# Performance work log

Hardware: AMD Instinct MI355X
Metric: run time of the kernel (lower is better)

## Reference

```python
import jax, jax.numpy as jnp
import numpy as np

T, H, I, E, K = 4096, 2048, 1408, 8, 2


def setup_inputs() -> dict:
    key = jax.random.key(0)
    k1, k2, k3, k4, k5 = jax.random.split(key, 5)
    hidden_states = jax.random.normal(k1, (T, H), dtype=jnp.float32)
    w13 = jax.random.normal(k2, (E, 2 * I, H), dtype=jnp.float32) * 0.02
    w2 = jax.random.normal(k3, (E, H, I), dtype=jnp.float32) * 0.02
    topk_ids = jax.random.randint(k4, (T, K), 0, E, dtype=jnp.int32)
    topk_weights = jax.random.uniform(k5, (T, K), dtype=jnp.float32)
    return {
        "hidden_states": hidden_states,
        "w13": w13,
        "w2": w2,
        "topk_ids": topk_ids,
        "topk_weights": topk_weights,
    }


def reference(hidden_states, w13, w2, topk_ids, topk_weights):
    # hidden_states: [T, H]; w13: [E, 2I, H]; w2: [E, H, I]
    # topk_ids/topk_weights: [T, K]. local_expert_start = 0.
    num_tokens, hidden = hidden_states.shape
    num_experts = w13.shape[0]
    inter = w13.shape[1] // 2
    gate_w = w13[:, :inter, :]  # [E, I, H]
    up_w = w13[:, inter:, :]    # [E, I, H]

    # Dense per-expert gate/up projections (vectorized grouped GEMM).
    gate = jnp.einsum('th,eih->tei', hidden_states, gate_w)
    up = jnp.einsum('th,eih->tei', hidden_states, up_w)
    act = jax.nn.silu(gate) * up  # [T, E, I]

    # Scatter topk weights into a dense [T, E] routing matrix (zero elsewhere),
    # which reproduces the trivial impl's per-slot weighted accumulation.
    tok = jnp.arange(num_tokens, dtype=jnp.int32)[:, None]
    routing = jnp.zeros((num_tokens, num_experts), dtype=hidden_states.dtype)
    routing = routing.at[tok, topk_ids].add(topk_weights)

    # Weighted combine through the down projection; weighting act first avoids
    # materializing a [T, E, H] intermediate.
    act_w = act * routing[:, :, None]  # [T, E, I]
    out = jnp.einsum('tei,ehi->th', act_w, w2)  # [T, H]
    return out
```

## Files before the change

kernel.cpp:

```cpp
#include <hip/hip_runtime.h>
#include <hip/hip_bf16.h>

#define T_TOK 4096
#define HID   2048
#define INTER 1408
#define TWO_I 2816
#define NEXP  8
#define ROWCAP 9216

#define N8_HS  1048576
#define N8_W13 5767168
#define NCVT   ((N8_HS + N8_W13) / 256)

#define NJOBS1 1408
#define NJOBS2 1024

using bf16x8 = __attribute__((ext_vector_type(8))) __bf16;
using f32x4  = __attribute__((ext_vector_type(4))) float;

__device__ __forceinline__ unsigned short f2bf(float f) {
  unsigned u = __float_as_uint(f);
  u += 0x7fffu + ((u >> 16) & 1u);
  return (unsigned short)(u >> 16);
}

__device__ __forceinline__ void gload16(const void* g, void* l) {
  __builtin_amdgcn_global_load_lds(
      (const __attribute__((address_space(1))) void*)g,
      (__attribute__((address_space(3))) void*)l, 16, 0, 0);
}

__device__ __forceinline__ uint4 pack8(float4 a, float4 b) {
  union { unsigned short us[8]; uint4 v; } o;
  o.us[0] = f2bf(a.x); o.us[1] = f2bf(a.y); o.us[2] = f2bf(a.z); o.us[3] = f2bf(a.w);
  o.us[4] = f2bf(b.x); o.us[5] = f2bf(b.y); o.us[6] = f2bf(b.z); o.us[7] = f2bf(b.w);
  return o.v;
}

__global__ void cvt2route_kernel(const float* __restrict__ hs_f, unsigned short* __restrict__ hs_b,
                                 const float* __restrict__ w13_f, unsigned short* __restrict__ w13_b,
                                 const int* __restrict__ ids, const float* __restrict__ wts,
                                 float* __restrict__ R, int* __restrict__ counts) {
  int bid = blockIdx.x;
  if (bid >= NCVT) {
    int t = (bid - NCVT) * 256 + threadIdx.x;
    if (t >= T_TOK) return;
    int e0 = ids[t * 2], e1 = ids[t * 2 + 1];
    float w0 = wts[t * 2], w1 = wts[t * 2 + 1];
#pragma unroll
    for (int ee = 0; ee < NEXP; ++ee) {
      float r = (e0 == ee ? w0 : 0.0f) + (e1 == ee ? w1 : 0.0f);
      R[t * NEXP + ee] = r;
    }
    atomicAdd(&counts[e0], 1);
    if (e1 != e0) atomicAdd(&counts[e1], 1);
    return;
  }
  int i = bid * 256 + threadIdx.x;
  const float4* p;
  uint4* o;
  int j;
  if (i < N8_HS) {
    p = reinterpret_cast<const float4*>(hs_f);
    o = reinterpret_cast<uint4*>(hs_b);
    j = i;
  } else {
    p = reinterpret_cast<const float4*>(w13_f);
    o = reinterpret_cast<uint4*>(w13_b);
    j = i - N8_HS;
  }
  o[j] = pack8(p[j * 2], p[j * 2 + 1]);
}

__global__ void offsets_kernel(const int* __restrict__ counts,
                               int* __restrict__ offs, int* __restrict__ cursor,
                               int* __restrict__ tl) {
  if (threadIdx.x == 0) {
    int o = 0;
    for (int e = 0; e < NEXP; ++e) {
      offs[e] = o;
      cursor[e] = o;
      o += (counts[e] + 127) & ~127;
    }
    offs[NEXP] = o;
  }
  for (int i = threadIdx.x; i < ROWCAP; i += 256) tl[i] = -1;
}

__global__ void scatter_kernel(const int* __restrict__ ids,
                               int* __restrict__ cursor, int* __restrict__ tl,
                               int* __restrict__ inv) {
  int t = blockIdx.x * 256 + threadIdx.x;
  if (t >= T_TOK) return;
  int e0 = ids[t * 2], e1 = ids[t * 2 + 1];
  int p = atomicAdd(&cursor[e0], 1);
  tl[p] = t;
  inv[t * 2] = p;
  if (e1 != e0) {
    p = atomicAdd(&cursor[e1], 1);
    tl[p] = t;
    inv[t * 2 + 1] = p;
  } else {
    inv[t * 2 + 1] = -1;
  }
}


#define BARR do { __asm__ __volatile__("" ::: "memory"); \
                  __builtin_amdgcn_s_barrier();           \
                  __asm__ __volatile__("" ::: "memory"); } while (0)
#define VMC(n) __asm__ __volatile__("s_waitcnt vmcnt(" #n ")" ::: "memory")

#define STG(P, h, kt, slotOff, hOff)                                        \
  do {                                                                      \
    gload16(P[h][0] + (kt) * 128, smem + (slotOff) + (hOff) + chA);         \
    gload16(P[h][1] + (kt) * 128, smem + (slotOff) + (hOff) + chA + 1024);  \
  } while (0)

#define LDA(dst, S, aq)                                                     \
  do {                                                                      \
    _Pragma("unroll") for (int mi = 0; mi < 4; ++mi) {                      \
      const char* _p = smem + (S) + wmOff + ((aq) * 64 + mi * 16 + l15) * 128; \
      dst[mi][0] = *(const bf16x8*)(_p + ko0);                              \
      dst[mi][1] = *(const bf16x8*)(_p + ko1);                              \
    }                                                                       \
  } while (0)

#define LDB(dst, S, bq)                                                     \
  do {                                                                      \
    _Pragma("unroll") for (int ni = 0; ni < 2; ++ni) {                      \
      const char* _p = smem + (S) + 32768 + wnhOff +                        \
                       (wn1 * 64 + ((bq) * 2 + ni) * 16 + l15) * 128;       \
      dst[ni][0] = *(const bf16x8*)(_p + ko0);                              \
      dst[ni][1] = *(const bf16x8*)(_p + ko1);                              \
    }                                                                       \
  } while (0)

#define MFQ(A, B, aq, bq)                                                   \
  do {                                                                      \
    __builtin_amdgcn_s_setprio(1);                                          \
    _Pragma("unroll") for (int mi = 0; mi < 4; ++mi)                        \
    _Pragma("unroll") for (int ni = 0; ni < 2; ++ni) {                      \
      acc[(aq) * 4 + mi][(bq) * 2 + ni] = __builtin_amdgcn_mfma_f32_16x16x32_bf16( \
          A[mi][0], B[ni][0], acc[(aq) * 4 + mi][(bq) * 2 + ni], 0, 0, 0);  \
      acc[(aq) * 4 + mi][(bq) * 2 + ni] = __builtin_amdgcn_mfma_f32_16x16x32_bf16( \
          A[mi][1], B[ni][1], acc[(aq) * 4 + mi][(bq) * 2 + ni], 0, 0, 0);  \
    }                                                                       \
    __builtin_amdgcn_s_setprio(0);                                          \
  } while (0)

#define EIGHT_PHASES(NIT_, NL_LIM_)                                         \
  for (int i = 0; i < (NIT_); ++i) {                                        \
    const int t0 = 2 * i, t1 = t0 + 1;                                      \
    const bool nl = (i < (NL_LIM_));                                        \
                                                                    \
    LDA(a_lo, 0, 0);                                                        \
    LDB(b_lo, 0, 0);                                                        \
    STG(aS, 0, t1, 65536, 0);                                               \
    BARR; MFQ(a_lo, b_lo, 0, 0); BARR;                                      \
                                                                    \
    LDB(b_hi, 0, 1);                                                        \
    STG(aS, 1, t1, 65536, 16384);                                           \
    BARR; MFQ(a_lo, b_hi, 0, 1); BARR;                                      \
                                                                    \
    LDA(a_hi, 0, 1);                                                        \
    if (nl) STG(bS, 0, t0 + 2, 0, 32768);                                   \
    BARR; MFQ(a_hi, b_hi, 1, 1); BARR;                                      \
                                                                    \
    if (nl) STG(bS, 1, t0 + 2, 0, 49152);                                   \
    BARR; MFQ(a_hi, b_lo, 1, 0);                                            \
    if (nl) { VMC(4); } else { VMC(0); }                                    \
    BARR;                                                                   \
                                                                    \
    LDA(a_lo, 65536, 0);                                                    \
    LDB(b_lo, 65536, 0);                                                    \
    if (nl) STG(aS, 0, t0 + 2, 0, 0);                                       \
    BARR; MFQ(a_lo, b_lo, 0, 0); BARR;                                      \
                                                                    \
    LDB(b_hi, 65536, 1);                                                    \
    if (nl) STG(aS, 1, t0 + 2, 0, 16384);                                   \
    BARR; MFQ(a_lo, b_hi, 0, 1); BARR;                                      \
                                                                    \
    LDA(a_hi, 65536, 1);                                                    \
    if (nl) STG(bS, 0, t1 + 2, 65536, 32768);                               \
    BARR; MFQ(a_hi, b_hi, 1, 1); BARR;                                      \
                                                                    \
    if (nl) STG(bS, 1, t1 + 2, 65536, 49152);                               \
    BARR; MFQ(a_hi, b_lo, 1, 0);                                            \
    if (nl) VMC(4);                                                         \
    BARR;                                                                   \
  }

#define PROLOGUE_STAGE()                                                    \
  do {                                                                      \
    STG(aS, 0, 0, 0, 0);                                                    \
    STG(aS, 1, 0, 0, 16384);                                                \
    STG(bS, 0, 0, 0, 32768);                                                \
    STG(bS, 1, 0, 0, 49152);                                                \
    STG(bS, 0, 1, 65536, 32768);                                            \
    STG(bS, 1, 1, 65536, 49152);                                            \
    VMC(4);                                                                 \
    BARR;                                                                   \
  } while (0)

__global__ __launch_bounds__(512, 2) void gemm1_kernel(
    const unsigned short* __restrict__ hs,
    const unsigned short* __restrict__ w13,
    unsigned short* __restrict__ act,
    const int* __restrict__ tl, const int* __restrict__ offs,
    const float* __restrict__ w2f, unsigned short* __restrict__ w2b,
    int* __restrict__ qcnt) {
  const int tid = threadIdx.x;

  {
    const float4* p = reinterpret_cast<const float4*>(w2f);
    uint4* o = reinterpret_cast<uint4*>(w2b);
    int gid = blockIdx.x * 512 + tid;
#pragma unroll
    for (int q = 0; q < 22; ++q) {
      int idx = q * 131072 + gid;
      o[idx] = pack8(p[idx * 2], p[idx * 2 + 1]);
    }
  }

  __shared__ __align__(16) char smem[131072];
  __shared__ int sjob;

  const int lane = tid & 63, wave = tid >> 6;
  const int wm = wave >> 2, wn = wave & 3;
  const int l15 = lane & 15;
  const int srow = lane >> 3;
  const int scolswz = ((lane & 7) * 16) ^ (srow << 4);
  const int chA = wave * 2048;
  const int wmOff = wm * 16384;
  const int wnhOff = (wn >> 1) * 16384;
  const int wn1 = wn & 1;
  const int rsw = (lane & 7) << 4;
  const int ko0 = ((lane >> 4) * 16) ^ rsw;
  const int ko1 = (64 + (lane >> 4) * 16) ^ rsw;

  const char* hs_b = (const char*)hs;

  for (;;) {
    if (tid == 0) sjob = atomicAdd(qcnt, 1);
    __syncthreads();
    const int job = sjob;
    __syncthreads();
    if (job >= NJOBS1) break;

    const int e = job / 176;
    const int rem = job - e * 176;
    const int by = rem / 11;
    const int bx = rem - by * 11;

    const int rbeg = offs[e], rend = offs[e + 1];
    const int m0 = rbeg + by * 256;
    if (m0 >= rend) continue;
    const int n0 = bx * 128;

    const char* w13_b = (const char*)w13 + (size_t)e * (TWO_I * HID * 2);

    const char* aS[2][2];
    const char* bS[2][2];
#pragma unroll
    for (int h = 0; h < 2; ++h)
#pragma unroll
      for (int it = 0; it < 2; ++it) {
        int rl = h * 128 + (wave * 2 + it) * 8 + srow;
        int grow = m0 + rl;
        int tk = (grow < rend) ? tl[grow] : 0;
        if (tk < 0) tk = 0;
        aS[h][it] = hs_b + (size_t)tk * 4096 + scolswz;
        int wg = rl >> 6, sub = rl & 63;
        int srcB = (sub < 32) ? (n0 + wg * 32 + sub)
                              : (INTER + n0 + wg * 32 + (sub - 32));
        bS[h][it] = w13_b + (size_t)srcB * 4096 + scolswz;
      }

    f32x4 acc[8][4] = {};
    bf16x8 a_lo[4][2], a_hi[4][2], b_lo[2][2], b_hi[2][2];

    PROLOGUE_STAGE();
    EIGHT_PHASES(16, 15);

    const bool okst = (wm == 0) || (rend - m0 >= 256);
    if (okst) {
#pragma unroll
      for (int MI = 0; MI < 8; ++MI)
#pragma unroll
        for (int j = 0; j < 4; ++j) {
          int row = m0 + wm * 128 + MI * 16 + (lane >> 4) * 4 + j;
          size_t base = (size_t)row * INTER + n0 + wn * 32;
#pragma unroll
          for (int NI = 0; NI < 2; ++NI) {
            float g = acc[MI][NI][j], u = acc[MI][NI + 2][j];
            float s = (g / (1.0f + __expf(-g))) * u;
            act[base + NI * 16 + l15] = f2bf(s);
          }
        }
    }
  }
}

__global__ __launch_bounds__(512, 2) void gemm2_kernel(
    const unsigned short* __restrict__ act,
    const unsigned short* __restrict__ w2,
    const float* __restrict__ R, const int* __restrict__ tl,
    const int* __restrict__ offs, unsigned short* __restrict__ partial,
    int* __restrict__ qcnt) {
  const int tid = threadIdx.x;

  __shared__ __align__(16) char smem[131072];
  __shared__ int sjob;

  const int lane = tid & 63, wave = tid >> 6;
  const int wm = wave >> 2, wn = wave & 3;
  const int l15 = lane & 15;
  const int srow = lane >> 3;
  const int scolswz = ((lane & 7) * 16) ^ (srow << 4);
  const int chA = wave * 2048;
  const int wmOff = wm * 16384;
  const int wnhOff = (wn >> 1) * 16384;
  const int wn1 = wn & 1;
  const int rsw = (lane & 7) << 4;
  const int ko0 = ((lane >> 4) * 16) ^ rsw;
  const int ko1 = (64 + (lane >> 4) * 16) ^ rsw;

  const char* act_b = (const char*)act;

  for (;;) {
    if (tid == 0) sjob = atomicAdd(qcnt, 1);
    __syncthreads();
    const int job = sjob;
    __syncthreads();
    if (job >= NJOBS2) break;

    const int e = job >> 7;
    const int rem = job & 127;
    const int by = rem >> 3;
    const int bx = rem & 7;

    const int rbeg = offs[e], rend = offs[e + 1];
    const int m0 = rbeg + by * 256;
    if (m0 >= rend) continue;
    const int n0 = bx * 256;

    const char* w2_b = (const char*)w2 + (size_t)e * (HID * INTER * 2);

    const char* aS[2][2];
    const char* bS[2][2];
#pragma unroll
    for (int h = 0; h < 2; ++h)
#pragma unroll
      for (int it = 0; it < 2; ++it) {
        int rl = h * 128 + (wave * 2 + it) * 8 + srow;
        int grow = m0 + rl;
        if (grow >= rend) grow = rbeg;
        aS[h][it] = act_b + (size_t)grow * (INTER * 2) + scolswz;
        bS[h][it] = w2_b + (size_t)(n0 + rl) * (INTER * 2) + scolswz;
      }

    f32x4 acc[8][4] = {};
    bf16x8 a_lo[4][2], a_hi[4][2], b_lo[2][2], b_hi[2][2];

    PROLOGUE_STAGE();
    EIGHT_PHASES(11, 10);

    const bool okst = (wm == 0) || (rend - m0 >= 256);
    if (okst) {
#pragma unroll
      for (int MI = 0; MI < 8; ++MI) {
        float sc[4];
#pragma unroll
        for (int j = 0; j < 4; ++j) {
          int row = m0 + wm * 128 + MI * 16 + (lane >> 4) * 4 + j;
          int t = tl[row];
          sc[j] = t >= 0 ? R[t * NEXP + e] : 0.0f;
        }
#pragma unroll
        for (int NI = 0; NI < 4; ++NI) {
          int col = n0 + wn * 64 + NI * 16 + l15;
#pragma unroll
          for (int j = 0; j < 4; ++j) {
            int row = m0 + wm * 128 + MI * 16 + (lane >> 4) * 4 + j;
            partial[(size_t)row * HID + col] = f2bf(acc[MI][NI][j] * sc[j]);
          }
        }
      }
    }
  }
}

__global__ void combine_kernel(const unsigned short* __restrict__ P,
                               const int* __restrict__ inv,
                               float* __restrict__ out) {
  int idx = blockIdx.x * 256 + threadIdx.x;
  int t = idx >> 8;
  int c = (idx & 255) << 3;
  int p0 = inv[t * 2], p1 = inv[t * 2 + 1];
  union { uint4 v; unsigned short us[8]; } a, b;
  a.v = *(const uint4*)(P + (size_t)p0 * HID + c);
  float f[8];
#pragma unroll
  for (int j = 0; j < 8; ++j) f[j] = __uint_as_float((unsigned)a.us[j] << 16);
  if (p1 >= 0) {
    b.v = *(const uint4*)(P + (size_t)p1 * HID + c);
#pragma unroll
    for (int j = 0; j < 8; ++j) f[j] += __uint_as_float((unsigned)b.us[j] << 16);
  }
  float4 lo = {f[0], f[1], f[2], f[3]}, hi = {f[4], f[5], f[6], f[7]};
  *(float4*)(out + (size_t)t * HID + c) = lo;
  *(float4*)(out + (size_t)t * HID + c + 4) = hi;
}

extern "C" void kernel_launch(void* const* d_in, const int* in_sizes, int n_in,
                              void* d_out, int out_size, void* d_ws, size_t ws_size,
                              hipStream_t stream) {
  const float* hs_f  = (const float*)d_in[0];
  const float* w13_f = (const float*)d_in[1];
  const float* w2_f  = (const float*)d_in[2];
  const int*   ids   = (const int*)d_in[3];
  const float* wts   = (const float*)d_in[4];
  float* out = (float*)d_out;
  char* ws = (char*)d_ws;

  unsigned short* hs_b  = (unsigned short*)(ws);
  unsigned short* w13_b = (unsigned short*)(ws + 16777216);
  unsigned short* w2_b  = (unsigned short*)(ws + 109051904);
  unsigned short* act   = (unsigned short*)(ws + 155189248);
  float* R              = (float*)(ws + 181141504);
  int*   tl             = (int*)(ws + 181272576);
  int*   inv            = (int*)(ws + 181309440);
  int*   meta           = (int*)(ws + 181342208);
  unsigned short* partial = (unsigned short*)(ws + 16777216);
  int* counts = meta;
  int* offs   = meta + 8;
  int* cursor = meta + 17;
  int* q1     = meta + 26;
  int* q2     = meta + 27;

  hipMemsetAsync(meta, 0, 32 * sizeof(int), stream);

  cvt2route_kernel<<<dim3(NCVT + 16), dim3(256), 0, stream>>>(
      hs_f, hs_b, w13_f, w13_b, ids, wts, R, counts);

  offsets_kernel<<<dim3(1), dim3(256), 0, stream>>>(counts, offs, cursor, tl);
  scatter_kernel<<<dim3(T_TOK / 256), dim3(256), 0, stream>>>(ids, cursor, tl, inv);

  gemm1_kernel<<<dim3(256), dim3(512), 0, stream>>>(hs_b, w13_b, act, tl, offs, w2_f, w2_b, q1);
  gemm2_kernel<<<dim3(256), dim3(512), 0, stream>>>(act, w2_b, R, tl, offs, partial, q2);
  combine_kernel<<<dim3(T_TOK * (HID / 8) / 256), dim3(256), 0, stream>>>(partial, inv, out);
}
```

Before: 356.3 us.

## Use per-expert work queues and defer w2 conversion to tail of gemm1

Replaces the single global job counter in both grouped GEMMs with eight per-expert queues sized from the actual routed row counts. Each block starts on the queue for its blockIdx and moves to the next expert once that queue is empty, so empty tiles are never dequeued and blocks sharing an expert reuse its weights in cache. The fp32-to-bf16 conversion of w2 moves from the start of gemm1 into a dynamically claimed tail loop, so blocks that finish GEMM work early fill the load-imbalance gap. Costs are extra atomics when a queue runs dry and w2 conversion possibly running late in gemm1.

```diff
diff --git a/kernel.cpp b/kernel.cpp
--- a/kernel.cpp
+++ b/kernel.cpp
@@ -12,8 +12,7 @@
 #define N8_W13 5767168
 #define NCVT   ((N8_HS + N8_W13) / 256)
 
-#define NJOBS1 1408
-#define NJOBS2 1024
+#define W2_CHUNKS 704
 
 using bf16x8 = __attribute__((ext_vector_type(8))) __bf16;
 using f32x4  = __attribute__((ext_vector_type(4))) float;
@@ -203,28 +202,39 @@
     BARR;                                                                   \
   } while (0)
 
+#define QPOP(QARR)                                                          \
+  do {                                                                      \
+    if (tid == 0) {                                                         \
+      int got = -1;                                                         \
+      while (qsel < 8) {                                                    \
+        int qe = (myx + qsel) & 7;                                          \
+        int j = atomicAdd(&QARR[qe], 1);                                    \
+        if (j < scap[qe]) { got = (qe << 8) | j; break; }                   \
+        ++qsel;                                                             \
+      }                                                                     \
+      sjob = got;                                                           \
+    }                                                                       \
+    __syncthreads();                                                        \
+  } while (0)
+
 __global__ __launch_bounds__(512, 2) void gemm1_kernel(
     const unsigned short* __restrict__ hs,
     const unsigned short* __restrict__ w13,
     unsigned short* __restrict__ act,
     const int* __restrict__ tl, const int* __restrict__ offs,
     const float* __restrict__ w2f, unsigned short* __restrict__ w2b,
-    int* __restrict__ qcnt) {
+    int* __restrict__ q1, int* __restrict__ qw2) {
   const int tid = threadIdx.x;
-
-  {
-    const float4* p = reinterpret_cast<const float4*>(w2f);
-    uint4* o = reinterpret_cast<uint4*>(w2b);
-    int gid = blockIdx.x * 512 + tid;
-#pragma unroll
-    for (int q = 0; q < 22; ++q) {
-      int idx = q * 131072 + gid;
-      o[idx] = pack8(p[idx * 2], p[idx * 2 + 1]);
-    }
-  }
 
   __shared__ __align__(16) char smem[131072];
   __shared__ int sjob;
+  __shared__ int scap[8];
+
+  if (tid < 8) {
+    int rb = offs[tid], re = offs[tid + 1];
+    scap[tid] = ((re - rb + 255) >> 8) * 11;
+  }
+  __syncthreads();
 
   const int lane = tid & 63, wave = tid >> 6;
   const int wm = wave >> 2, wn = wave & 3;
@@ -240,22 +250,22 @@
   const int ko1 = (64 + (lane >> 4) * 16) ^ rsw;
 
   const char* hs_b = (const char*)hs;
+  const int myx = blockIdx.x & 7;
+  int qsel = 0;
 
   for (;;) {
-    if (tid == 0) sjob = atomicAdd(qcnt, 1);
-    __syncthreads();
+    QPOP(q1);
     const int job = sjob;
     __syncthreads();
-    if (job >= NJOBS1) break;
-
-    const int e = job / 176;
-    const int rem = job - e * 176;
-    const int by = rem / 11;
-    const int bx = rem - by * 11;
+    if (job < 0) break;
+
+    const int e = job >> 8;
+    const int j = job & 255;
+    const int by = j / 11;
+    const int bx = j - by * 11;
 
     const int rbeg = offs[e], rend = offs[e + 1];
     const int m0 = rbeg + by * 256;
-    if (m0 >= rend) continue;
     const int n0 = bx * 128;
 
     const char* w13_b = (const char*)w13 + (size_t)e * (TWO_I * HID * 2);
@@ -288,18 +298,35 @@
 #pragma unroll
       for (int MI = 0; MI < 8; ++MI)
 #pragma unroll
-        for (int j = 0; j < 4; ++j) {
-          int row = m0 + wm * 128 + MI * 16 + (lane >> 4) * 4 + j;
+        for (int j2 = 0; j2 < 4; ++j2) {
+          int row = m0 + wm * 128 + MI * 16 + (lane >> 4) * 4 + j2;
           size_t base = (size_t)row * INTER + n0 + wn * 32;
 #pragma unroll
           for (int NI = 0; NI < 2; ++NI) {
-            float g = acc[MI][NI][j], u = acc[MI][NI + 2][j];
+            float g = acc[MI][NI][j2], u = acc[MI][NI + 2][j2];
             float s = (g / (1.0f + __expf(-g))) * u;
             act[base + NI * 16 + l15] = f2bf(s);
           }
         }
     }
   }
+
+  {
+    const float4* p = reinterpret_cast<const float4*>(w2f);
+    uint4* o = reinterpret_cast<uint4*>(w2b);
+    for (;;) {
+      if (tid == 0) sjob = atomicAdd(qw2, 1);
+      __syncthreads();
+      int c = sjob;
+      __syncthreads();
+      if (c >= W2_CHUNKS) break;
+#pragma unroll
+      for (int k = 0; k < 8; ++k) {
+        int idx = c * 4096 + k * 512 + tid;
+        o[idx] = pack8(p[idx * 2], p[idx * 2 + 1]);
+      }
+    }
+  }
 }
 
 __global__ __launch_bounds__(512, 2) void gemm2_kernel(
@@ -307,11 +334,18 @@
     const unsigned short* __restrict__ w2,
     const float* __restrict__ R, const int* __restrict__ tl,
     const int* __restrict__ offs, unsigned short* __restrict__ partial,
-    int* __restrict__ qcnt) {
+    int* __restrict__ q2) {
   const int tid = threadIdx.x;
 
   __shared__ __align__(16) char smem[131072];
   __shared__ int sjob;
+  __shared__ int scap[8];
+
+  if (tid < 8) {
+    int rb = offs[tid], re = offs[tid + 1];
+    scap[tid] = ((re - rb + 255) >> 8) * 8;
+  }
+  __syncthreads();
 
   const int lane = tid & 63, wave = tid >> 6;
   const int wm = wave >> 2, wn = wave & 3;
@@ -327,22 +361,22 @@
   const int ko1 = (64 + (lane >> 4) * 16) ^ rsw;
 
   const char* act_b = (const char*)act;
+  const int myx = blockIdx.x & 7;
+  int qsel = 0;
 
   for (;;) {
-    if (tid == 0) sjob = atomicAdd(qcnt, 1);
-    __syncthreads();
+    QPOP(q2);
     const int job = sjob;
     __syncthreads();
-    if (job >= NJOBS2) break;
-
-    const int e = job >> 7;
-    const int rem = job & 127;
-    const int by = rem >> 3;
-    const int bx = rem & 7;
+    if (job < 0) break;
+
+    const int e = job >> 8;
+    const int j = job & 255;
+    const int by = j >> 3;
+    const int bx = j & 7;
 
     const int rbeg = offs[e], rend = offs[e + 1];
     const int m0 = rbeg + by * 256;
-    if (m0 >= rend) continue;
     const int n0 = bx * 256;
 
     const char* w2_b = (const char*)w2 + (size_t)e * (HID * INTER * 2);
@@ -372,18 +406,18 @@
       for (int MI = 0; MI < 8; ++MI) {
         float sc[4];
 #pragma unroll
-        for (int j = 0; j < 4; ++j) {
-          int row = m0 + wm * 128 + MI * 16 + (lane >> 4) * 4 + j;
+        for (int j2 = 0; j2 < 4; ++j2) {
+          int row = m0 + wm * 128 + MI * 16 + (lane >> 4) * 4 + j2;
           int t = tl[row];
-          sc[j] = t >= 0 ? R[t * NEXP + e] : 0.0f;
+          sc[j2] = t >= 0 ? R[t * NEXP + e] : 0.0f;
         }
 #pragma unroll
         for (int NI = 0; NI < 4; ++NI) {
           int col = n0 + wn * 64 + NI * 16 + l15;
 #pragma unroll
-          for (int j = 0; j < 4; ++j) {
-            int row = m0 + wm * 128 + MI * 16 + (lane >> 4) * 4 + j;
-            partial[(size_t)row * HID + col] = f2bf(acc[MI][NI][j] * sc[j]);
+          for (int j2 = 0; j2 < 4; ++j2) {
+            int row = m0 + wm * 128 + MI * 16 + (lane >> 4) * 4 + j2;
+            partial[(size_t)row * HID + col] = f2bf(acc[MI][NI][j2] * sc[j2]);
           }
         }
       }
@@ -436,10 +470,11 @@
   int* counts = meta;
   int* offs   = meta + 8;
   int* cursor = meta + 17;
-  int* q1     = meta + 26;
-  int* q2     = meta + 27;
-
-  hipMemsetAsync(meta, 0, 32 * sizeof(int), stream);
+  int* q1     = meta + 25;
+  int* q2     = meta + 33;
+  int* qw2    = meta + 41;
+
+  hipMemsetAsync(meta, 0, 48 * sizeof(int), stream);
 
   cvt2route_kernel<<<dim3(NCVT + 16), dim3(256), 0, stream>>>(
       hs_f, hs_b, w13_f, w13_b, ids, wts, R, counts);
@@ -447,7 +482,7 @@
   offsets_kernel<<<dim3(1), dim3(256), 0, stream>>>(counts, offs, cursor, tl);
   scatter_kernel<<<dim3(T_TOK / 256), dim3(256), 0, stream>>>(ids, cursor, tl, inv);
 
-  gemm1_kernel<<<dim3(256), dim3(512), 0, stream>>>(hs_b, w13_b, act, tl, offs, w2_f, w2_b, q1);
+  gemm1_kernel<<<dim3(256), dim3(512), 0, stream>>>(hs_b, w13_b, act, tl, offs, w2_f, w2_b, q1, qw2);
   gemm2_kernel<<<dim3(256), dim3(512), 0, stream>>>(act, w2_b, R, tl, offs, partial, q2);
   combine_kernel<<<dim3(T_TOK * (HID / 8) / 256), dim3(256), 0, stream>>>(partial, inv, out);
 }
```

Result: no change. 349.4 us (-1.9%).
